# Kernel tuning notes

Hardware: AMD Instinct MI355X
Metric: run time of the kernel (lower is better)

## Reference

```python
import jax, jax.numpy as jnp
import numpy as np

N = 50000      # nodes
E = 800000     # edges (avg degree 16)
B = 128        # graphs in batch
F_IN = 30      # raw node feature dim
PORT_DIM = 32
FLAG_DIM = 2
H = 64         # hidden_dim; also F_IN+PORT_DIM+FLAG_DIM = 64
L = 3          # number of GraphConv layers
C = 10         # num_classes
TOTAL_PORTS = 65536
TCP_FLAGS_VALUES = 256


def setup_inputs() -> dict:
    key = jax.random.key(0)
    ks = jax.random.split(key, 20)
    s = 0.1  # weight init scale
    return {
        "x": jax.random.normal(ks[0], (N, F_IN), jnp.float32),
        "dst_ports": jax.random.randint(ks[1], (N,), 0, TOTAL_PORTS, jnp.int64),
        "tcp_flags": jax.random.randint(ks[2], (N,), 0, TCP_FLAGS_VALUES, jnp.int64),
        "edge_index": jax.random.randint(ks[3], (2, E), 0, N, jnp.int64),
        "batch": jnp.sort(jax.random.randint(ks[4], (N,), 0, B, jnp.int64)),
        # learned parameters
        "emb_port": jax.random.normal(ks[5], (TOTAL_PORTS, PORT_DIM), jnp.float32) * s,
        "emb_flags": jax.random.normal(ks[6], (TCP_FLAGS_VALUES, FLAG_DIM), jnp.float32) * s,
        "Wrel": jax.random.normal(ks[7], (L, H, H), jnp.float32) * s,   # lin_rel weight (out,in)
        "brel": jax.random.normal(ks[8], (L, H), jnp.float32) * s,      # lin_rel bias
        "Wroot": jax.random.normal(ks[9], (L, H, H), jnp.float32) * s,  # lin_root weight, no bias
        "fc1_W": jax.random.normal(ks[10], (H, H), jnp.float32) * s,
        "fc1_b": jax.random.normal(ks[11], (H,), jnp.float32) * s,
        "fc2_W": jax.random.normal(ks[12], (H, H), jnp.float32) * s,
        "fc2_b": jax.random.normal(ks[13], (H,), jnp.float32) * s,
        "fc3_W": jax.random.normal(ks[14], (C, H), jnp.float32) * s,
        "fc3_b": jax.random.normal(ks[15], (C,), jnp.float32) * s,
    }


def reference(x, dst_ports, tcp_flags, edge_index, batch,
              emb_port, emb_flags, Wrel, brel, Wroot,
              fc1_W, fc1_b, fc2_W, fc2_b, fc3_W, fc3_b):
    # embedding lookups + concat -> [N, 64]
    h = jnp.concatenate([x, emb_port[dst_ports], emb_flags[tcp_flags]], axis=1)
    src, dst = edge_index[0], edge_index[1]
    # PyG GraphConv (aggr='add'): h' = lin_rel(sum_{j->i} h_j) + lin_root(h_i)
    for l in range(L):
        agg = jax.ops.segment_sum(h[src], dst, num_segments=N)  # gather + scatter-add
        h = agg @ Wrel[l].T + brel[l] + h @ Wroot[l].T
        h = jax.nn.relu(h)  # dropout inactive (eval mode)
    # global_max_pool over graphs -> [B, H]
    g = jax.ops.segment_max(h, batch, num_segments=B)
    # MLP head (dropout inactive)
    g = jax.nn.relu(g @ fc1_W.T + fc1_b)
    g = jax.nn.relu(g @ fc2_W.T + fc2_b)
    return g @ fc3_W.T + fc3_b
```

## Files before the change

kernel.cpp:

```cpp
#include <hip/hip_runtime.h>

#define NN 50000
#define NE 800000
#define NB 128
#define FIN 30
#define H 64
#define NC 10
#define L 3

#define BKN 4
#define NBK 12500
#define BKCAP 128
#define BSTRIDE 16

typedef unsigned int uint;
typedef unsigned short ushort;
typedef __attribute__((ext_vector_type(8))) short bf16x8;
typedef __attribute__((ext_vector_type(4))) float f32x4;

__device__ __forceinline__ ushort f2bf(float x) {
    uint u = __float_as_uint(x);
    u += 0x7fffu + ((u >> 16) & 1u);
    return (ushort)(u >> 16);
}
__device__ __forceinline__ float bf_lo(uint v) { return __uint_as_float(v << 16); }
__device__ __forceinline__ float bf_hi(uint v) { return __uint_as_float(v & 0xffff0000u); }


__global__ __launch_bounds__(256) void prep_weights_kernel(
    const float* __restrict__ Wrel, const float* __restrict__ Wroot,
    ushort* __restrict__ Wb, int* __restrict__ bcnt)
{
    int t = blockIdx.x * 256 + threadIdx.x;
    for (int i = t; i < NBK * BSTRIDE; i += 96 * 256) bcnt[i] = 0;
    if (t >= L * 2 * H * H) return;
    int l = t / (2 * H * H), rem = t % (2 * H * H);
    int mat = rem / (H * H), jk = rem % (H * H);
    const float* W = mat ? Wroot : Wrel;
    Wb[t] = f2bf(W[l * H * H + jk]);
}

__global__ __launch_bounds__(256) void bucketA_kernel(
    const int* __restrict__ src, const int* __restrict__ dst,
    int* __restrict__ bcnt, int2* __restrict__ tmp)
{
    int e = blockIdx.x * 256 + threadIdx.x;
    if (e >= NE) return;
    int d = dst[e];
    int b = d >> 2;
    int pos = atomicAdd(&bcnt[b * BSTRIDE], 1);
    if (pos < BKCAP) tmp[(size_t)b * BKCAP + pos] = make_int2(d & 3, src[e] << 7);
}

__global__ __launch_bounds__(64) void bucketB_kernel(
    const int2* __restrict__ tmp, const int* __restrict__ bcnt,
    int* __restrict__ edge_arr, int2* __restrict__ node_range)
{
    __shared__ int cnt[BKN];
    __shared__ int off[BKN];
    __shared__ int cur[BKN];
    int b = blockIdx.x;
    int tid = threadIdx.x;
    int ec = bcnt[b * BSTRIDE]; if (ec > BKCAP) ec = BKCAP;
    const int2* te = tmp + (size_t)b * BKCAP;

    if (tid < BKN) cnt[tid] = 0;
    __syncthreads();
    for (int t = tid; t < ec; t += 64) atomicAdd(&cnt[te[t].x], 1);
    __syncthreads();
    if (tid == 0) {
        int s = 0;
#pragma unroll
        for (int i = 0; i < BKN; ++i) { off[i] = s; cur[i] = s; s += cnt[i]; }
    }
    __syncthreads();
    for (int t = tid; t < ec; t += 64) {
        int2 ed = te[t];
        int p = atomicAdd(&cur[ed.x], 1);
        edge_arr[(size_t)b * BKCAP + p] = ed.y;
    }
    if (tid < BKN) {
        int n = b * BKN + tid;
        if (n < NN) node_range[n] = make_int2(b * BKCAP + off[tid], cnt[tid]);
    }
}

__global__ __launch_bounds__(256) void gemm0_fused_kernel(
    const float* __restrict__ x, const int* __restrict__ ports,
    const int* __restrict__ flags, const float* __restrict__ emb_port,
    const float* __restrict__ emb_flags,
    const ushort* __restrict__ Wb, const float* __restrict__ brel,
    ushort* __restrict__ z0, ushort* __restrict__ z1)
{
    __shared__ float sf[64 * 65];
    __shared__ float so[64 * 65];
    int tid = threadIdx.x, lane = tid & 63, w = tid >> 6;
    int node0 = blockIdx.x * 64;

    for (int t = tid; t < 4096; t += 256) {
        int r = t >> 6, f = t & 63;
        int n = node0 + r;
        float v = 0.f;
        if (n < NN) {
            if (f < FIN)       v = x[(size_t)n * FIN + f];
            else if (f < 62)   v = emb_port[(size_t)ports[n] * 32 + (f - FIN)];
            else               v = emb_flags[(size_t)flags[n] * 2 + (f - 62)];
        }
        sf[r * 65 + f] = v;
    }
    __syncthreads();

    int m  = lane & 15;
    int kg = lane >> 4;
    int rloc = w * 16 + m;
    const float* fr = &sf[rloc * 65 + kg * 8];
    bf16x8 a0, a1;
#pragma unroll
    for (int i = 0; i < 8; ++i) {
        a0[i] = (short)f2bf(fr[i]);
        a1[i] = (short)f2bf(fr[32 + i]);
    }

    f32x4 acc0[4], acc1[4];
#pragma unroll
    for (int jt = 0; jt < 4; ++jt) {
        const ushort* wr0 = Wb + ((size_t)(jt * 16 + m)) * 64 + kg * 8;
        const ushort* wr1 = wr0 + (size_t)H * H;
        bf16x8 b00 = *(const bf16x8*)(wr0);
        bf16x8 b01 = *(const bf16x8*)(wr0 + 32);
        bf16x8 b10 = *(const bf16x8*)(wr1);
        bf16x8 b11 = *(const bf16x8*)(wr1 + 32);
        float bias = brel[jt * 16 + m];
        acc0[jt] = f32x4{0.f, 0.f, 0.f, 0.f};
        acc1[jt] = f32x4{bias, bias, bias, bias};
        acc0[jt] = __builtin_amdgcn_mfma_f32_16x16x32_bf16(a0, b00, acc0[jt], 0, 0, 0);
        acc0[jt] = __builtin_amdgcn_mfma_f32_16x16x32_bf16(a1, b01, acc0[jt], 0, 0, 0);
        acc1[jt] = __builtin_amdgcn_mfma_f32_16x16x32_bf16(a0, b10, acc1[jt], 0, 0, 0);
        acc1[jt] = __builtin_amdgcn_mfma_f32_16x16x32_bf16(a1, b11, acc1[jt], 0, 0, 0);
    }

    int nl = w * 16 + kg * 4;

#pragma unroll
    for (int jt = 0; jt < 4; ++jt)
#pragma unroll
        for (int r = 0; r < 4; ++r)
            so[(nl + r) * 65 + jt * 16 + m] = acc0[jt][r];
    __syncthreads();
    for (int t = tid; t < 512; t += 256) {
        int rr = t >> 3, oct = t & 7;
        if (node0 + rr < NN) {
            const float* s = &so[rr * 65 + oct * 8];
            uint4 v;
            v.x = (uint)f2bf(s[0]) | ((uint)f2bf(s[1]) << 16);
            v.y = (uint)f2bf(s[2]) | ((uint)f2bf(s[3]) << 16);
            v.z = (uint)f2bf(s[4]) | ((uint)f2bf(s[5]) << 16);
            v.w = (uint)f2bf(s[6]) | ((uint)f2bf(s[7]) << 16);
            *((uint4*)(z0 + (size_t)node0 * H) + t) = v;
        }
    }
    __syncthreads();

#pragma unroll
    for (int jt = 0; jt < 4; ++jt)
#pragma unroll
        for (int r = 0; r < 4; ++r)
            so[(nl + r) * 65 + jt * 16 + m] = acc1[jt][r];
    __syncthreads();
    for (int t = tid; t < 512; t += 256) {
        int rr = t >> 3, oct = t & 7;
        if (node0 + rr < NN) {
            const float* s = &so[rr * 65 + oct * 8];
            uint4 v;
            v.x = (uint)f2bf(s[0]) | ((uint)f2bf(s[1]) << 16);
            v.y = (uint)f2bf(s[2]) | ((uint)f2bf(s[3]) << 16);
            v.z = (uint)f2bf(s[4]) | ((uint)f2bf(s[5]) << 16);
            v.w = (uint)f2bf(s[6]) | ((uint)f2bf(s[7]) << 16);
            *((uint4*)(z1 + (size_t)node0 * H) + t) = v;
        }
    }
}

__global__ __launch_bounds__(256) void gemm_kernel(
    const ushort* __restrict__ h_in, const ushort* __restrict__ Wb,
    const float* __restrict__ brel,
    ushort* __restrict__ z0, ushort* __restrict__ z1)
{
    __shared__ float so[64 * 65];
    int tid = threadIdx.x, lane = tid & 63, w = tid >> 6;
    int m  = lane & 15;
    int kg = lane >> 4;
    int node0 = blockIdx.x * 64 + w * 16;

    int row = node0 + m; if (row >= NN) row = NN - 1;
    const ushort* hr = h_in + (size_t)row * H + kg * 8;
    bf16x8 a0 = *(const bf16x8*)(hr);
    bf16x8 a1 = *(const bf16x8*)(hr + 32);

    f32x4 acc0[4], acc1[4];
#pragma unroll
    for (int jt = 0; jt < 4; ++jt) {
        const ushort* wr0 = Wb + ((size_t)(jt * 16 + m)) * 64 + kg * 8;
        const ushort* wr1 = wr0 + (size_t)H * H;
        bf16x8 b00 = *(const bf16x8*)(wr0);
        bf16x8 b01 = *(const bf16x8*)(wr0 + 32);
        bf16x8 b10 = *(const bf16x8*)(wr1);
        bf16x8 b11 = *(const bf16x8*)(wr1 + 32);
        float bias = brel[jt * 16 + m];
        acc0[jt] = f32x4{0.f, 0.f, 0.f, 0.f};
        acc1[jt] = f32x4{bias, bias, bias, bias};
        acc0[jt] = __builtin_amdgcn_mfma_f32_16x16x32_bf16(a0, b00, acc0[jt], 0, 0, 0);
        acc0[jt] = __builtin_amdgcn_mfma_f32_16x16x32_bf16(a1, b01, acc0[jt], 0, 0, 0);
        acc1[jt] = __builtin_amdgcn_mfma_f32_16x16x32_bf16(a0, b10, acc1[jt], 0, 0, 0);
        acc1[jt] = __builtin_amdgcn_mfma_f32_16x16x32_bf16(a1, b11, acc1[jt], 0, 0, 0);
    }

    int nl = w * 16 + kg * 4;
    int nodeS0 = blockIdx.x * 64;

#pragma unroll
    for (int jt = 0; jt < 4; ++jt)
#pragma unroll
        for (int r = 0; r < 4; ++r)
            so[(nl + r) * 65 + jt * 16 + m] = acc0[jt][r];
    __syncthreads();
    for (int t = tid; t < 512; t += 256) {
        int rr = t >> 3, oct = t & 7;
        if (nodeS0 + rr < NN) {
            const float* s = &so[rr * 65 + oct * 8];
            uint4 v;
            v.x = (uint)f2bf(s[0]) | ((uint)f2bf(s[1]) << 16);
            v.y = (uint)f2bf(s[2]) | ((uint)f2bf(s[3]) << 16);
            v.z = (uint)f2bf(s[4]) | ((uint)f2bf(s[5]) << 16);
            v.w = (uint)f2bf(s[6]) | ((uint)f2bf(s[7]) << 16);
            *((uint4*)(z0 + (size_t)nodeS0 * H) + t) = v;
        }
    }
    __syncthreads();

#pragma unroll
    for (int jt = 0; jt < 4; ++jt)
#pragma unroll
        for (int r = 0; r < 4; ++r)
            so[(nl + r) * 65 + jt * 16 + m] = acc1[jt][r];
    __syncthreads();
    for (int t = tid; t < 512; t += 256) {
        int rr = t >> 3, oct = t & 7;
        if (nodeS0 + rr < NN) {
            const float* s = &so[rr * 65 + oct * 8];
            uint4 v;
            v.x = (uint)f2bf(s[0]) | ((uint)f2bf(s[1]) << 16);
            v.y = (uint)f2bf(s[2]) | ((uint)f2bf(s[3]) << 16);
            v.z = (uint)f2bf(s[4]) | ((uint)f2bf(s[5]) << 16);
            v.w = (uint)f2bf(s[6]) | ((uint)f2bf(s[7]) << 16);
            *((uint4*)(z1 + (size_t)nodeS0 * H) + t) = v;
        }
    }
}

__global__ __launch_bounds__(256) void gather_relu_kernel(
    const ushort* __restrict__ z0, const ushort* __restrict__ z1,
    const int2* __restrict__ node_range, const int* __restrict__ edge_arr,
    ushort* __restrict__ h_out)
{
    int tid = blockIdx.x * 256 + threadIdx.x;
    int n = tid >> 3, oct = tid & 7;
    if (n >= NN) return;
    int2 rng = node_range[n];
    int p0 = rng.x, p1 = rng.x + rng.y;
    const char* zb = (const char*)z0 + oct * 16;
    float a[8] = {0.f,0.f,0.f,0.f,0.f,0.f,0.f,0.f};
    for (int p = p0; p < p1; p += 8) {
        bool g[8]; int o[8]; uint4 v[8];
#pragma unroll
        for (int q = 0; q < 8; ++q) {
            g[q] = (p + q) < p1;
            o[q] = g[q] ? edge_arr[p + q] : 0;
        }
#pragma unroll
        for (int q = 0; q < 8; ++q) {
            v[q] = make_uint4(0u, 0u, 0u, 0u);
            if (g[q]) v[q] = *(const uint4*)(zb + o[q]);
        }
#pragma unroll
        for (int q = 0; q < 8; ++q) {
            a[0] += bf_lo(v[q].x); a[1] += bf_hi(v[q].x);
            a[2] += bf_lo(v[q].y); a[3] += bf_hi(v[q].y);
            a[4] += bf_lo(v[q].z); a[5] += bf_hi(v[q].z);
            a[6] += bf_lo(v[q].w); a[7] += bf_hi(v[q].w);
        }
    }
    uint4 sv = *(const uint4*)((const char*)z1 + (size_t)n * 128 + oct * 16);
    a[0] += bf_lo(sv.x); a[1] += bf_hi(sv.x);
    a[2] += bf_lo(sv.y); a[3] += bf_hi(sv.y);
    a[4] += bf_lo(sv.z); a[5] += bf_hi(sv.z);
    a[6] += bf_lo(sv.w); a[7] += bf_hi(sv.w);
    uint4 o;
    o.x = (uint)f2bf(fmaxf(a[0], 0.f)) | ((uint)f2bf(fmaxf(a[1], 0.f)) << 16);
    o.y = (uint)f2bf(fmaxf(a[2], 0.f)) | ((uint)f2bf(fmaxf(a[3], 0.f)) << 16);
    o.z = (uint)f2bf(fmaxf(a[4], 0.f)) | ((uint)f2bf(fmaxf(a[5], 0.f)) << 16);
    o.w = (uint)f2bf(fmaxf(a[6], 0.f)) | ((uint)f2bf(fmaxf(a[7], 0.f)) << 16);
    *((uint4*)h_out + tid) = o;
}

__global__ __launch_bounds__(256) void pool_mlp_kernel(
    const ushort* __restrict__ h, const int* __restrict__ batch,
    const float* __restrict__ fc1W, const float* __restrict__ fc1b,
    const float* __restrict__ fc2W, const float* __restrict__ fc2b,
    const float* __restrict__ fc3W, const float* __restrict__ fc3b,
    float* __restrict__ out)
{
    __shared__ float red[4][64];
    __shared__ float s0[64];
    __shared__ float s1[64];
    __shared__ float s2[64];
    int b = blockIdx.x;
    int tid = threadIdx.x;
    int f = tid & 63, w = tid >> 6;
    int lo = 0, hi = NN;
    while (lo < hi) { int mid = (lo + hi) >> 1; if (batch[mid] < b) lo = mid + 1; else hi = mid; }
    int lo2 = lo, hi2 = NN;
    while (lo2 < hi2) { int mid = (lo2 + hi2) >> 1; if (batch[mid] < b + 1) lo2 = mid + 1; else hi2 = mid; }
    float m = -3.402823466e38f;
    for (int n = lo + w; n < lo2; n += 4) {
        ushort u = h[(size_t)n * H + f];
        m = fmaxf(m, __uint_as_float((uint)u << 16));
    }
    red[w][f] = m;
    __syncthreads();
    int j = tid;
    if (tid < 64)
        s0[j] = fmaxf(fmaxf(red[0][j], red[1][j]), fmaxf(red[2][j], red[3][j]));
    __syncthreads();
    float acc = 0.f;
    if (tid < 64) {
        acc = fc1b[j];
        for (int k = 0; k < 64; ++k) acc = fmaf(s0[k], fc1W[j * 64 + k], acc);
    }
    __syncthreads();
    if (tid < 64) s1[j] = fmaxf(acc, 0.f);
    __syncthreads();
    if (tid < 64) {
        acc = fc2b[j];
        for (int k = 0; k < 64; ++k) acc = fmaf(s1[k], fc2W[j * 64 + k], acc);
    }
    __syncthreads();
    if (tid < 64) s2[j] = fmaxf(acc, 0.f);
    __syncthreads();
    if (tid < NC) {
        acc = fc3b[j];
        for (int k = 0; k < 64; ++k) acc = fmaf(s2[k], fc3W[j * 64 + k], acc);
        out[b * NC + j] = acc;
    }
}


extern "C" void kernel_launch(void* const* d_in, const int* in_sizes, int n_in,
                              void* d_out, int out_size, void* d_ws, size_t ws_size,
                              hipStream_t stream)
{
    const float* x         = (const float*)d_in[0];
    const int*   dst_ports = (const int*)d_in[1];
    const int*   tcp_flags = (const int*)d_in[2];
    const int*   edge_src_in = (const int*)d_in[3];
    const int*   edge_dst_in = edge_src_in + NE;
    const int*   batch     = (const int*)d_in[4];
    const float* emb_port  = (const float*)d_in[5];
    const float* emb_flags = (const float*)d_in[6];
    const float* Wrel      = (const float*)d_in[7];
    const float* brel      = (const float*)d_in[8];
    const float* Wroot     = (const float*)d_in[9];
    const float* fc1W      = (const float*)d_in[10];
    const float* fc1b      = (const float*)d_in[11];
    const float* fc2W      = (const float*)d_in[12];
    const float* fc2b      = (const float*)d_in[13];
    const float* fc3W      = (const float*)d_in[14];
    const float* fc3b      = (const float*)d_in[15];
    float* out = (float*)d_out;

    char* ws = (char*)d_ws;
    size_t off = 0;
    auto alloc = [&](size_t bytes) {
        void* p = ws + off;
        off += (bytes + 255) & ~(size_t)255;
        return p;
    };
    ushort* hA        = (ushort*)alloc((size_t)NN * H * 2);
    ushort* hB        = (ushort*)alloc((size_t)NN * H * 2);
    ushort* z0        = (ushort*)alloc((size_t)NN * H * 2);
    ushort* z1        = (ushort*)alloc((size_t)NN * H * 2);
    int2*   tmp       = (int2*)alloc((size_t)NBK * BKCAP * 8);
    int*    edge_arr  = (int*)alloc((size_t)NBK * BKCAP * 4);
    int2*   node_range= (int2*)alloc((size_t)NN * 8);
    int*    bcnt      = (int*)alloc((size_t)NBK * BSTRIDE * 4);
    ushort* Wb        = (ushort*)alloc((size_t)L * 2 * H * H * 2);

    prep_weights_kernel<<<96, 256, 0, stream>>>(Wrel, Wroot, Wb, bcnt);

    bucketA_kernel<<<(NE + 255) / 256, 256, 0, stream>>>(edge_src_in, edge_dst_in, bcnt, tmp);
    bucketB_kernel<<<NBK, 64, 0, stream>>>(tmp, bcnt, edge_arr, node_range);

    const int ggrid = (NN + 63) / 64;
    const int agrid = (NN * 8 + 255) / 256;
    gemm0_fused_kernel<<<ggrid, 256, 0, stream>>>(
        x, dst_ports, tcp_flags, emb_port, emb_flags, Wb, brel, z0, z1);
    gather_relu_kernel<<<agrid, 256, 0, stream>>>(z0, z1, node_range, edge_arr, hA);

    gemm_kernel<<<ggrid, 256, 0, stream>>>(
        hA, Wb + (size_t)1 * 2 * H * H, brel + 1 * H, z0, z1);
    gather_relu_kernel<<<agrid, 256, 0, stream>>>(z0, z1, node_range, edge_arr, hB);
    gemm_kernel<<<ggrid, 256, 0, stream>>>(
        hB, Wb + (size_t)2 * 2 * H * H, brel + 2 * H, z0, z1);
    gather_relu_kernel<<<agrid, 256, 0, stream>>>(z0, z1, node_range, edge_arr, hA);

    pool_mlp_kernel<<<NB, 256, 0, stream>>>(
        hA, batch, fc1W, fc1b, fc2W, fc2b, fc3W, fc3b, out);
}
```

Measured before the change: 292.3 us.

## Replace global-atomic edge bucketing with counting-sort CSR build via prefix scan

Replaces the per-edge global atomic bucketing into fixed-capacity 4-node buckets with a two-level counting sort. Per-block LDS histograms over 128-node buckets are scanned globally, edges are scattered to exact offsets, and each bucket is then sorted by node in shared memory. This removes contended global atomics and the padded, strided bucket arrays, and drops the 128-edge per-4-node capacity limit in favour of an exact CSR. The cost is several extra kernel launches for the scan, and a per-bucket LDS capacity of 2816 edges that silently truncates a bucket with more incoming edges.

Result: faster. 272.3 us (-6.9%).

```diff
diff --git a/kernel.cpp b/kernel.cpp
--- a/kernel.cpp
+++ b/kernel.cpp
@@ -8,10 +8,11 @@
 #define NC 10
 #define L 3
 
-#define BKN 4
-#define NBK 12500
-#define BKCAP 128
-#define BSTRIDE 16
+#define EBS 2048
+#define NEB 391
+#define NBX 391
+#define NS (NBX * NEB)
+#define SECAP 2816
 
 typedef unsigned int uint;
 typedef unsigned short ushort;
@@ -29,10 +30,9 @@
 
 __global__ __launch_bounds__(256) void prep_weights_kernel(
     const float* __restrict__ Wrel, const float* __restrict__ Wroot,
-    ushort* __restrict__ Wb, int* __restrict__ bcnt)
+    ushort* __restrict__ Wb)
 {
     int t = blockIdx.x * 256 + threadIdx.x;
-    for (int i = t; i < NBK * BSTRIDE; i += 96 * 256) bcnt[i] = 0;
     if (t >= L * 2 * H * H) return;
     int l = t / (2 * H * H), rem = t % (2 * H * H);
     int mat = rem / (H * H), jk = rem % (H * H);
@@ -40,48 +40,138 @@
     Wb[t] = f2bf(W[l * H * H + jk]);
 }
 
-__global__ __launch_bounds__(256) void bucketA_kernel(
+__global__ __launch_bounds__(256) void count_kernel(
+    const int* __restrict__ dst, int* __restrict__ counts)
+{
+    __shared__ int cnt[NBX];
+    int eb = blockIdx.x, tid = threadIdx.x;
+    for (int t = tid; t < NBX; t += 256) cnt[t] = 0;
+    __syncthreads();
+#pragma unroll
+    for (int q = 0; q < 8; ++q) {
+        int e = eb * EBS + q * 256 + tid;
+        if (e < NE) atomicAdd(&cnt[dst[e] >> 7], 1);
+    }
+    __syncthreads();
+    for (int t = tid; t < NBX; t += 256) counts[t * NEB + eb] = cnt[t];
+}
+
+__global__ __launch_bounds__(1024) void scanA1_kernel(
+    const int* __restrict__ counts, int* __restrict__ offs, int* __restrict__ bsum)
+{
+    __shared__ int wsum[16];
+    int i = blockIdx.x * 1024 + threadIdx.x;
+    int lane = threadIdx.x & 63;
+    int wv = threadIdx.x >> 6;
+    int v = (i < NS) ? counts[i] : 0;
+    int s = v;
+    for (int off = 1; off < 64; off <<= 1) {
+        int t = __shfl_up(s, off);
+        if (lane >= off) s += t;
+    }
+    if (lane == 63) wsum[wv] = s;
+    __syncthreads();
+    if (wv == 0) {
+        int ws = (lane < 16) ? wsum[lane] : 0;
+        for (int off = 1; off < 16; off <<= 1) {
+            int t = __shfl_up(ws, off);
+            if (lane >= off) ws += t;
+        }
+        if (lane < 16) wsum[lane] = ws;
+    }
+    __syncthreads();
+    int base = (wv > 0) ? wsum[wv - 1] : 0;
+    s += base;
+    if (i < NS) offs[i] = s - v;
+    if (threadIdx.x == 1023) bsum[blockIdx.x] = s;
+}
+
+__global__ __launch_bounds__(256) void scanA2_kernel(int* __restrict__ bsum, int nblk)
+{
+    __shared__ int arr[256];
+    int t = threadIdx.x;
+    int v = (t < nblk) ? bsum[t] : 0;
+    arr[t] = v;
+    __syncthreads();
+    for (int off = 1; off < 256; off <<= 1) {
+        int u = (t >= off) ? arr[t - off] : 0;
+        __syncthreads();
+        arr[t] += u;
+        __syncthreads();
+    }
+    if (t < nblk) bsum[t] = arr[t] - v;
+}
+
+__global__ __launch_bounds__(1024) void scanA3_kernel(
+    int* __restrict__ offs, const int* __restrict__ bsum)
+{
+    int b = blockIdx.x + 1;
+    int i = b * 1024 + threadIdx.x;
+    if (i < NS) offs[i] += bsum[b];
+}
+
+__global__ __launch_bounds__(256) void scatter_ranked_kernel(
     const int* __restrict__ src, const int* __restrict__ dst,
-    int* __restrict__ bcnt, int2* __restrict__ tmp)
-{
-    int e = blockIdx.x * 256 + threadIdx.x;
-    if (e >= NE) return;
-    int d = dst[e];
-    int b = d >> 2;
-    int pos = atomicAdd(&bcnt[b * BSTRIDE], 1);
-    if (pos < BKCAP) tmp[(size_t)b * BKCAP + pos] = make_int2(d & 3, src[e] << 7);
-}
-
-__global__ __launch_bounds__(64) void bucketB_kernel(
-    const int2* __restrict__ tmp, const int* __restrict__ bcnt,
+    const int* __restrict__ offs, int* __restrict__ tmp)
+{
+    __shared__ int cur[NBX];
+    int eb = blockIdx.x, tid = threadIdx.x;
+    for (int t = tid; t < NBX; t += 256) cur[t] = offs[t * NEB + eb];
+    __syncthreads();
+#pragma unroll
+    for (int q = 0; q < 8; ++q) {
+        int e = eb * EBS + q * 256 + tid;
+        if (e < NE) {
+            int d = dst[e];
+            int b = d >> 7;
+            int pos = atomicAdd(&cur[b], 1);
+            tmp[pos] = (src[e] << 7) | (d & 127);
+        }
+    }
+}
+
+__global__ __launch_bounds__(256) void bucket_sort_kernel(
+    const int* __restrict__ tmp, const int* __restrict__ offs,
     int* __restrict__ edge_arr, int2* __restrict__ node_range)
 {
-    __shared__ int cnt[BKN];
-    __shared__ int off[BKN];
-    __shared__ int cur[BKN];
-    int b = blockIdx.x;
-    int tid = threadIdx.x;
-    int ec = bcnt[b * BSTRIDE]; if (ec > BKCAP) ec = BKCAP;
-    const int2* te = tmp + (size_t)b * BKCAP;
-
-    if (tid < BKN) cnt[tid] = 0;
-    __syncthreads();
-    for (int t = tid; t < ec; t += 64) atomicAdd(&cnt[te[t].x], 1);
-    __syncthreads();
-    if (tid == 0) {
-        int s = 0;
-#pragma unroll
-        for (int i = 0; i < BKN; ++i) { off[i] = s; cur[i] = s; s += cnt[i]; }
-    }
-    __syncthreads();
-    for (int t = tid; t < ec; t += 64) {
-        int2 ed = te[t];
-        int p = atomicAdd(&cur[ed.x], 1);
-        edge_arr[(size_t)b * BKCAP + p] = ed.y;
-    }
-    if (tid < BKN) {
-        int n = b * BKN + tid;
-        if (n < NN) node_range[n] = make_int2(b * BKCAP + off[tid], cnt[tid]);
+    __shared__ int se[SECAP];
+    __shared__ int cnt[128];
+    __shared__ int off[128];
+    __shared__ int cur[128];
+    int b = blockIdx.x, tid = threadIdx.x;
+    int start = offs[b * NEB];
+    int end   = (b + 1 < NBX) ? offs[(b + 1) * NEB] : NE;
+    int ec = end - start; if (ec > SECAP) ec = SECAP;
+
+    if (tid < 128) cnt[tid] = 0;
+    __syncthreads();
+    for (int t = tid; t < ec; t += 256) {
+        int v = tmp[start + t];
+        se[t] = v;
+        atomicAdd(&cnt[v & 127], 1);
+    }
+    __syncthreads();
+    if (tid < 64) {
+        int v0 = cnt[2 * tid], v1 = cnt[2 * tid + 1];
+        int s = v0 + v1;
+        for (int o = 1; o < 64; o <<= 1) {
+            int t = __shfl_up(s, o);
+            if (tid >= o) s += t;
+        }
+        off[2 * tid]     = s - v1 - v0;
+        off[2 * tid + 1] = s - v1;
+        cur[2 * tid]     = s - v1 - v0;
+        cur[2 * tid + 1] = s - v1;
+    }
+    __syncthreads();
+    for (int t = tid; t < ec; t += 256) {
+        int v = se[t];
+        int p = atomicAdd(&cur[v & 127], 1);
+        edge_arr[start + p] = v & ~127;
+    }
+    if (tid < 128) {
+        int n = b * 128 + tid;
+        if (n < NN) node_range[n] = make_int2(start + off[tid], cnt[tid]);
     }
 }
 
@@ -389,16 +479,23 @@
     ushort* hB        = (ushort*)alloc((size_t)NN * H * 2);
     ushort* z0        = (ushort*)alloc((size_t)NN * H * 2);
     ushort* z1        = (ushort*)alloc((size_t)NN * H * 2);
-    int2*   tmp       = (int2*)alloc((size_t)NBK * BKCAP * 8);
-    int*    edge_arr  = (int*)alloc((size_t)NBK * BKCAP * 4);
+    int*    counts    = (int*)alloc((size_t)NS * 4);
+    int*    tmp       = (int*)alloc((size_t)NE * 4);
+    int*    edge_arr  = (int*)alloc((size_t)NE * 4);
     int2*   node_range= (int2*)alloc((size_t)NN * 8);
-    int*    bcnt      = (int*)alloc((size_t)NBK * BSTRIDE * 4);
+    int*    bsum      = (int*)alloc((size_t)256 * 4);
     ushort* Wb        = (ushort*)alloc((size_t)L * 2 * H * H * 2);
 
-    prep_weights_kernel<<<96, 256, 0, stream>>>(Wrel, Wroot, Wb, bcnt);
-
-    bucketA_kernel<<<(NE + 255) / 256, 256, 0, stream>>>(edge_src_in, edge_dst_in, bcnt, tmp);
-    bucketB_kernel<<<NBK, 64, 0, stream>>>(tmp, bcnt, edge_arr, node_range);
+    const int SBLK = (NS + 1023) / 1024;
+
+    prep_weights_kernel<<<96, 256, 0, stream>>>(Wrel, Wroot, Wb);
+
+    count_kernel<<<NEB, 256, 0, stream>>>(edge_dst_in, counts);
+    scanA1_kernel<<<SBLK, 1024, 0, stream>>>(counts, counts, bsum);
+    scanA2_kernel<<<1, 256, 0, stream>>>(bsum, SBLK);
+    scanA3_kernel<<<SBLK - 1, 1024, 0, stream>>>(counts, bsum);
+    scatter_ranked_kernel<<<NEB, 256, 0, stream>>>(edge_src_in, edge_dst_in, counts, tmp);
+    bucket_sort_kernel<<<NBX, 256, 0, stream>>>(tmp, counts, edge_arr, node_range);
 
     const int ggrid = (NN + 63) / 64;
     const int agrid = (NN * 8 + 255) / 256;
```
